# Kernel tuning notes

Measured on AMD Instinct MI355X. Metric: run time of the kernel, lower is better.

The kernel has to match this reference:

```python
import jax, jax.numpy as jnp
import numpy as np

T, N, C, S = 1600, 32, 512, 200
BLANK = 0
ALPHA = 0.5
NEG = -1e30  # finite stand-in for -inf (safe for grads)


def setup_inputs() -> dict:
    key = jax.random.key(0)
    k1, k2, k3 = jax.random.split(key, 3)
    # valid log-probabilities (log-softmax over vocab), shape (T, N, C)
    log_probs = jax.nn.log_softmax(jax.random.normal(k1, (T, N, C), jnp.float32), axis=-1)
    # labels in [1, C) so blank=0 never appears in targets
    targets = jax.random.randint(k2, (N, S), 1, C)
    input_lens = jnp.full((N,), T, dtype=jnp.int32)
    target_lens = jax.random.randint(k3, (N,), S // 2, S + 1)
    return {"log_probs": log_probs, "targets": targets,
            "input_lens": input_lens, "target_lens": target_lens}


def _ctc_forward(log_probs, targets, input_lens, target_lens):
    """Per-example CTC negative log-likelihood (reduction='none')."""
    Tt, Nn, Cc = log_probs.shape
    Ss = targets.shape[1]
    L = 2 * Ss + 1  # extended label sequence: blank, l1, blank, l2, ...

    ext = jnp.zeros((Nn, L), dtype=targets.dtype).at[:, 1::2].set(targets)  # (N, L)
    s_idx = jnp.arange(L)
    ext_m2 = jnp.pad(ext, ((0, 0), (2, 0)), constant_values=BLANK)[:, :L]
    # skip transition s-2 -> s allowed only for non-blank labels differing from s-2
    allow_skip = (ext != BLANK) & (ext != ext_m2) & (s_idx >= 2)[None, :]

    emit0 = jnp.take_along_axis(log_probs[0], ext, axis=1)  # (N, L)
    alpha0 = jnp.full((Nn, L), NEG, jnp.float32)
    alpha0 = alpha0.at[:, 0].set(emit0[:, 0])
    alpha0 = alpha0.at[:, 1].set(jnp.where(target_lens >= 1, emit0[:, 1], NEG))

    def step(alpha, xs):
        lp_t, t = xs  # lp_t: (N, C)
        emit = jnp.take_along_axis(lp_t, ext, axis=1)  # (N, L)
        a1 = jnp.pad(alpha, ((0, 0), (1, 0)), constant_values=NEG)[:, :L]
        a2 = jnp.where(allow_skip,
                       jnp.pad(alpha, ((0, 0), (2, 0)), constant_values=NEG)[:, :L],
                       NEG)
        m = jnp.maximum(jnp.maximum(alpha, a1), a2)
        new = m + jnp.log(jnp.exp(alpha - m) + jnp.exp(a1 - m) + jnp.exp(a2 - m)) + emit
        active = (t < input_lens)[:, None]  # freeze trellis past input_len
        return jnp.where(active, new, alpha), None

    alpha, _ = jax.lax.scan(step, alpha0, (log_probs[1:], jnp.arange(1, Tt)))

    idx_last = (2 * target_lens).astype(jnp.int32)  # final blank position
    idx_prev = jnp.maximum(idx_last - 1, 0)  # final label position
    a_last = jnp.take_along_axis(alpha, idx_last[:, None], axis=1)[:, 0]
    a_prev = jnp.where(target_lens > 0,
                       jnp.take_along_axis(alpha, idx_prev[:, None], axis=1)[:, 0],
                       NEG)
    return -jnp.logaddexp(a_last, a_prev)  # (N,)


def reference(log_probs, targets, input_lens, target_lens):
    per_ex = _ctc_forward(log_probs, targets, input_lens, target_lens)
    # zero_infinity=True: zero out infeasible alignments
    per_ex = jnp.where(per_ex < 1e29, per_ex, 0.0)
    norm = jnp.maximum(target_lens.astype(jnp.float32), 1.0) ** ALPHA
    return jnp.mean(per_ex / norm)
```

## Files before the change

kernel.cpp:

```cpp
#include <hip/hip_runtime.h>

#define T_DIM 1600
#define N_DIM 32
#define C_DIM 512
#define S_DIM 200
#define RCP_LN2 1.44269504088896340736f
#define LN2F 0.69314718055994530942f
#define ESENT (-(1 << 28))

static __device__ __forceinline__ float fast_exp2(float x) {
#if __has_builtin(__builtin_amdgcn_exp2f)
    return __builtin_amdgcn_exp2f(x);
#else
    return exp2f(x);
#endif
}

static __device__ __forceinline__ float fast_log2(float x) {
#if __has_builtin(__builtin_amdgcn_logf)
    return __builtin_amdgcn_logf(x);
#else
    return log2f(x);
#endif
}

static __device__ __forceinline__ float dpp_shr1_f(float x) {
    return __int_as_float(__builtin_amdgcn_update_dpp(
        0, __float_as_int(x), 0x138, 0xf, 0xf, false));
}
static __device__ __forceinline__ int dpp_shr1_i(int x, int old0) {
    return __builtin_amdgcn_update_dpp(old0, x, 0x138, 0xf, 0xf, false);
}
static __device__ __forceinline__ int dpp_prefix_max_i(int x) {
    int t;
    t = __builtin_amdgcn_update_dpp(x, x, 0x111, 0xf, 0xf, false); x = (t > x) ? t : x;
    t = __builtin_amdgcn_update_dpp(x, x, 0x112, 0xf, 0xf, false); x = (t > x) ? t : x;
    t = __builtin_amdgcn_update_dpp(x, x, 0x114, 0xf, 0xf, false); x = (t > x) ? t : x;
    t = __builtin_amdgcn_update_dpp(x, x, 0x118, 0xf, 0xf, false); x = (t > x) ? t : x;
    t = __builtin_amdgcn_update_dpp(x, x, 0x142, 0xf, 0xf, false); x = (t > x) ? t : x;
    t = __builtin_amdgcn_update_dpp(x, x, 0x143, 0xf, 0xf, false); x = (t > x) ? t : x;
    return x;
}

static __device__ __forceinline__ void gl_lds16(const float* g, float* l) {
    __builtin_amdgcn_global_load_lds(
        (const __attribute__((address_space(1))) unsigned int*)g,
        (__attribute__((address_space(3))) unsigned int*)l, 16, 0, 0);
}

#define VMWAIT16() __builtin_amdgcn_s_waitcnt(0x4F70)

__global__ __launch_bounds__(64) void ctc_dp(
    const float* __restrict__ lp, const int* __restrict__ tgts,
    const int* __restrict__ input_lens, const int* __restrict__ target_lens,
    float* __restrict__ out, float* __restrict__ ws)
{
    __shared__ float rows[3][8][C_DIM];

    const int blk = blockIdx.x;
    const int n = blk >> 1;
    const int role = blk & 1;
    const int lane = threadIdx.x & 63;
    const int* tgt = tgts + n * S_DIM;

    int len = input_lens[n];
    if (len > T_DIM) len = T_DIM;
    const int lenc = (len < 1) ? 1 : len;
    const int tl = target_lens[n];
    const int mid = (lenc + 1) >> 1;
    const int nsb = lenc - mid;

    float* afin_g = ws + 64 + (size_t)n * 1152;
    float* bfin_g = afin_g + 512;
    int* escF_g = (int*)(afin_g + 1024);
    int* escB_g = escF_g + 64;
    int* counter = (int*)ws + n;

#define TMAP_F(ti_) ((ti_) > mid - 1 ? mid - 1 : (ti_))
#define TMAP_B(ti_) (lenc - 1 - (ti_) < 0 ? 0 : lenc - 1 - (ti_))

#define ISSUE(B_, c_, TMAP_) do {                                             \
        int tb_ = (c_) * 8;                                                   \
        _Pragma("unroll")                                                     \
        for (int r_ = 0; r_ < 8; ++r_) {                                      \
            int ti_ = tb_ + r_;                                               \
            int t_ = TMAP_(ti_);                                              \
            const float* g_ = lp + ((size_t)t_ * N_DIM + n) * C_DIM + lane*4; \
            gl_lds16(g_,       &rows[(B_)][r_][0]);                           \
            gl_lds16(g_ + 256, &rows[(B_)][r_][256]);                         \
        }                                                                     \
    } while (0)

#define GATHER_RAW(B_, LAB_, qb_, q1_, q3_, q5_, q7_) do {                    \
        _Pragma("unroll")                                                     \
        for (int r_ = 0; r_ < 8; ++r_) {                                      \
            qb_[r_] = rows[(B_)][r_][0];                                      \
            q1_[r_] = rows[(B_)][r_][LAB_[0]];                                \
            q3_[r_] = rows[(B_)][r_][LAB_[1]];                                \
            q5_[r_] = rows[(B_)][r_][LAB_[2]];                                \
            q7_[r_] = rows[(B_)][r_][LAB_[3]];                                \
        }                                                                     \
    } while (0)

#define BOUNDARY() do {                                                       \
        float lm_ = fmaxf(fmaxf(fmaxf(a0, a1), fmaxf(a2, a3)),                \
                          fmaxf(fmaxf(a4, a5), fmaxf(a6, a7)));               \
        bool nz_ = (lm_ > 0.0f);                                              \
        int kl_ = (int)((__float_as_uint(lm_) >> 23) & 0xffu) - 127;          \
        int prop_ = nz_ ? (E + kl_) : ESENT;                                  \
        int g_ = dpp_prefix_max_i(prop_ + 32 * lane);                         \
        int Efin_ = g_ - 32 * lane;                                           \
        if (nz_) {                                                            \
            int sh_ = E - Efin_;                                              \
            int h1_ = sh_ / 2, h2_ = sh_ - h1_;                               \
            float f_ = fast_exp2((float)h1_), gg_ = fast_exp2((float)h2_);    \
            float fg_ = f_ * gg_;                                             \
            a0 *= fg_; a1 *= fg_; a2 *= fg_; a3 *= fg_;                       \
            a4 *= fg_; a5 *= fg_; a6 *= fg_; a7 *= fg_;                       \
        }                                                                     \
        int Eprev_ = dpp_shr1_i(Efin_, ESENT);                                \
        E = Efin_;                                                            \
        if (lane == 0) {                                                      \
            scale_d = 0.0f;                                                   \
        } else {                                                              \
            int d_ = Eprev_ - Efin_;               \
            scale_d = (d_ < -126) ? 0.0f : fast_exp2((float)d_);              \
        }                                                                     \
    } while (0)

#define COMPUTE_F(c8_, FIRST_, qb_, q1_, q3_, q5_, q7_) do {                  \
        _Pragma("unroll")                                                     \
        for (int r_ = 0; r_ < 8; ++r_) {                                      \
            int t_ = (c8_) + r_;                                              \
            if (t_ >= mid) break;                                             \
            float pb_ = fast_exp2(qb_[r_] * RCP_LN2);                         \
            float p1_ = fast_exp2(q1_[r_] * RCP_LN2);                         \
            float p3_ = fast_exp2(q3_[r_] * RCP_LN2);                         \
            float p5_ = fast_exp2(q5_[r_] * RCP_LN2);                         \
            float p7_ = fast_exp2(q7_[r_] * RCP_LN2);                         \
            if ((FIRST_) && r_ == 0) {                                        \
                if (lane == 0) {                                              \
                    a0 = pb_;                                                 \
                    a1 = (tl >= 1) ? p1_ : 0.0f;                              \
                }                                                             \
            } else {                                                          \
                float P_ = dpp_shr1_f(a7) * scale_d;                          \
                float n0_ = (a0 + P_) * pb_;                                  \
                float n1_ = fmaf(sk[0], P_,  a1 + a0) * p1_;                  \
                float n2_ = (a2 + a1) * pb_;                                  \
                float n3_ = fmaf(sk[1], a1, a3 + a2) * p3_;                   \
                float n4_ = (a4 + a3) * pb_;                                  \
                float n5_ = fmaf(sk[2], a3, a5 + a4) * p5_;                   \
                float n6_ = (a6 + a5) * pb_;                                  \
                float n7_ = fmaf(sk[3], a5, a7 + a6) * p7_;                   \
                a0 = n0_; a1 = n1_; a2 = n2_; a3 = n3_;                       \
                a4 = n4_; a5 = n5_; a6 = n6_; a7 = n7_;                       \
            }                                                                 \
        }                                                                     \
    } while (0)

#define COMPUTE_B(c8_, qb_, q1_, q3_, q5_, q7_) do {                          \
        _Pragma("unroll")                                                     \
        for (int r_ = 0; r_ < 8; ++r_) {                                      \
            int ti_ = (c8_) + r_;                                             \
            if (ti_ >= nsb) break;                                            \
            float pb_ = fast_exp2(qb_[r_] * RCP_LN2);                         \
            float p1_ = fast_exp2(q1_[r_] * RCP_LN2);                         \
            float p3_ = fast_exp2(q3_[r_] * RCP_LN2);                         \
            float p5_ = fast_exp2(q5_[r_] * RCP_LN2);                         \
            float p7_ = fast_exp2(q7_[r_] * RCP_LN2);                         \
            float c0_ = pb_ * a0, c1_ = p1_ * a1;                             \
            float c2_ = pb_ * a2, c3_ = p3_ * a3;                             \
            float c4_ = pb_ * a4, c5_ = p5_ * a5;                             \
            float c6_ = pb_ * a6, c7_ = p7_ * a7;                             \
            float P_ = dpp_shr1_f(c7_) * scale_d;                             \
            a0 = c0_ + P_;                                                    \
            a1 = fmaf(aH[0], P_,  c1_ + c0_);                                 \
            a2 = c2_ + c1_;                                                   \
            a3 = fmaf(aH[1], c1_, c3_ + c2_);                                 \
            a4 = c4_ + c3_;                                                   \
            a5 = fmaf(aH[2], c3_, c5_ + c4_);                                 \
            a6 = c6_ + c5_;                                                   \
            a7 = fmaf(aH[3], c5_, c7_ + c6_);                                 \
        }                                                                     \
    } while (0)

#define PHASE_F(k_, GB_, GS_, CS_, IB_, F_) do {                              \
        VMWAIT16();                                                           \
        GATHER_RAW(GB_, labidx, qb##GS_, q1##GS_, q3##GS_, q5##GS_, q7##GS_); \
        COMPUTE_F((k_) * 8, F_, qb##CS_, q1##CS_, q3##CS_, q5##CS_, q7##CS_); \
        BOUNDARY();                                                           \
        ISSUE(IB_, (k_) + 3, TMAP_F);                                         \
    } while (0)

#define PHASE_B(k_, GB_, GS_, CS_, IB_) do {                                  \
        VMWAIT16();                                                           \
        GATHER_RAW(GB_, labH, qb##GS_, q1##GS_, q3##GS_, q5##GS_, q7##GS_);   \
        COMPUTE_B((k_) * 8, qb##CS_, q1##CS_, q3##CS_, q5##CS_, q7##CS_);     \
        BOUNDARY();                                                           \
        ISSUE(IB_, (k_) + 3, TMAP_B);                                         \
    } while (0)

    if (role == 0) {
        int labidx[4];
        float sk[4];
#pragma unroll
        for (int jj = 0; jj < 4; ++jj) {
            int s = lane * 8 + 2 * jj + 1;
            int i = (s - 1) >> 1;
            int lab = 0;
            float al = 0.0f;
            if (i < S_DIM) {
                lab = tgt[i];
                if (s >= 3 && i >= 1) al = (tgt[i] != tgt[i - 1]) ? 1.0f : 0.0f;
            }
            if (lab < 0 || lab >= C_DIM) lab = 0;
            labidx[jj] = lab;
            sk[jj] = al;
        }

        float a0 = 0.0f, a1 = 0.0f, a2 = 0.0f, a3 = 0.0f;
        float a4 = 0.0f, a5 = 0.0f, a6 = 0.0f, a7 = 0.0f;
        int E = 0;
        float scale_d = (lane == 0) ? 0.0f : 1.0f;
        float qbA[8], q1A[8], q3A[8], q5A[8], q7A[8];
        float qbB[8], q1B[8], q3B[8], q5B[8], q7B[8];

        ISSUE(0, 0, TMAP_F);
        ISSUE(1, 1, TMAP_F);
        VMWAIT16();
        GATHER_RAW(0, labidx, qbA, q1A, q3A, q5A, q7A);
        ISSUE(2, 2, TMAP_F);

        const int ncf = (mid + 7) >> 3;
        const int kmaxf = ((ncf + 5) / 6) * 6;
        for (int k6 = 0; k6 < kmaxf; k6 += 6) {
            bool f0 = (k6 == 0);
            PHASE_F(k6 + 0, 1, B, A, 0, f0);
            PHASE_F(k6 + 1, 2, A, B, 1, false);
            PHASE_F(k6 + 2, 0, B, A, 2, false);
            PHASE_F(k6 + 3, 1, A, B, 0, false);
            PHASE_F(k6 + 4, 2, B, A, 1, false);
            PHASE_F(k6 + 5, 0, A, B, 2, false);
        }

        float4 lo = make_float4(a0, a1, a2, a3);
        float4 hi = make_float4(a4, a5, a6, a7);
        reinterpret_cast<float4*>(afin_g)[lane * 2] = lo;
        reinterpret_cast<float4*>(afin_g)[lane * 2 + 1] = hi;
        escF_g[lane] = E;
    } else {
        int labH[4];
        float aH[4];
#pragma unroll
        for (int jj = 0; jj < 4; ++jj) {
            int shat = lane * 8 + 2 * jj + 1;
            int s = 510 - shat;
            int lab = 0;
            float al = 0.0f;
            if (s >= 1 && s <= 399) {
                lab = tgt[(s - 1) >> 1];
                if (s + 2 <= 400) al = (tgt[(s + 1) >> 1] != tgt[(s - 1) >> 1]) ? 1.0f : 0.0f;
            }
            if (lab < 0 || lab >= C_DIM) lab = 0;
            labH[jj] = lab;
            aH[jj] = al;
        }

        float a0, a1, a2, a3, a4, a5, a6, a7;
#define BINIT(aj_, j_) do {                                                   \
            int s_ = 510 - (lane * 8 + (j_));                                 \
            aj_ = (s_ == 2 * tl || (tl > 0 && s_ == 2 * tl - 1)) ? 1.0f : 0.0f; \
        } while (0)
        BINIT(a0, 0); BINIT(a1, 1); BINIT(a2, 2); BINIT(a3, 3);
        BINIT(a4, 4); BINIT(a5, 5); BINIT(a6, 6); BINIT(a7, 7);
#undef BINIT
        int E = 0;
        float scale_d = (lane == 0) ? 0.0f : 1.0f;
        float qbA[8], q1A[8], q3A[8], q5A[8], q7A[8];
        float qbB[8], q1B[8], q3B[8], q5B[8], q7B[8];

        ISSUE(0, 0, TMAP_B);
        ISSUE(1, 1, TMAP_B);
        VMWAIT16();
        GATHER_RAW(0, labH, qbA, q1A, q3A, q5A, q7A);
        ISSUE(2, 2, TMAP_B);

        const int ncb = (nsb + 7) >> 3;
        const int kmaxb = ((ncb + 5) / 6) * 6;
        for (int k6 = 0; k6 < kmaxb; k6 += 6) {
            PHASE_B(k6 + 0, 1, B, A, 0);
            PHASE_B(k6 + 1, 2, A, B, 1);
            PHASE_B(k6 + 2, 0, B, A, 2);
            PHASE_B(k6 + 3, 1, A, B, 0);
            PHASE_B(k6 + 4, 2, B, A, 1);
            PHASE_B(k6 + 5, 0, A, B, 2);
        }

        float4 lo = make_float4(a0, a1, a2, a3);
        float4 hi = make_float4(a4, a5, a6, a7);
        reinterpret_cast<float4*>(bfin_g)[lane * 2] = lo;
        reinterpret_cast<float4*>(bfin_g)[lane * 2 + 1] = hi;
        escB_g[lane] = E;
    }

    __threadfence();
    int prev = 0;
    if (lane == 0)
        prev = __hip_atomic_fetch_add(counter, 1, __ATOMIC_ACQ_REL,
                                      __HIP_MEMORY_SCOPE_AGENT);
    prev = __shfl(prev, 0);
    if (prev != 1) return;

    __threadfence();

    {
        const int l = lane;
        const int Ef = escF_g[l];
        float m8 = -1e30f, s8 = 0.0f;
#pragma unroll
        for (int j = 0; j < 8; ++j) {
            int s = 8 * l + j;
            float x = -1e30f;
            if (s <= 400) {
                float af = afin_g[s];
                int shat = 510 - s;
                float bf = bfin_g[shat];
                if (af > 0.0f && bf > 0.0f)
                    x = fast_log2(af) + fast_log2(bf) + (float)(Ef + escB_g[shat >> 3]);
            }
            float m2 = fmaxf(m8, x);
            s8 = s8 * fast_exp2(m8 - m2) + fast_exp2(x - m2);
            m8 = m2;
        }
        float M = m8, V = s8;
#pragma unroll
        for (int off = 1; off < 64; off <<= 1) {
            float Mo = __shfl_xor(M, off);
            float Vo = __shfl_xor(V, off);
            float Mn = fmaxf(M, Mo);
            V = V * fast_exp2(M - Mn) + Vo * fast_exp2(Mo - Mn);
            M = Mn;
        }
        if (l == 0) {
            float X = M + fast_log2(V);
            float per_ex = -LN2F * X;
            if (!(per_ex < 1e29f)) per_ex = 0.0f;
            float tlf = (float)tl;
            if (tlf < 1.0f) tlf = 1.0f;
            atomicAdd(out, per_ex / sqrtf(tlf) * (1.0f / N_DIM));
        }
    }
#undef ISSUE
#undef GATHER_RAW
#undef BOUNDARY
#undef COMPUTE_F
#undef COMPUTE_B
#undef PHASE_F
#undef PHASE_B
#undef TMAP_F
#undef TMAP_B
}

extern "C" void kernel_launch(void* const* d_in, const int* in_sizes, int n_in,
                              void* d_out, int out_size, void* d_ws, size_t ws_size,
                              hipStream_t stream) {
    (void)in_sizes; (void)n_in; (void)ws_size;
    const float* lp   = (const float*)d_in[0];
    const int* tgts   = (const int*)d_in[1];
    const int* ilens  = (const int*)d_in[2];
    const int* tlens  = (const int*)d_in[3];

    hipMemsetAsync(d_out, 0, (size_t)out_size * sizeof(float), stream);
    hipMemsetAsync(d_ws, 0, N_DIM * sizeof(int), stream);
    ctc_dp<<<2 * N_DIM, 64, 0, stream>>>(lp, tgts, ilens, tlens,
                                         (float*)d_out, (float*)d_ws);
}
```

Baseline: 248.8 us.

## Split CTC recurrence into producer and consumer wavefronts with LDS handoff

```diff
diff --git a/kernel.cpp b/kernel.cpp
--- a/kernel.cpp
+++ b/kernel.cpp
@@ -48,19 +48,29 @@
         (__attribute__((address_space(3))) unsigned int*)l, 16, 0, 0);
 }
 
-#define VMWAIT16() __builtin_amdgcn_s_waitcnt(0x4F70)
-
-__global__ __launch_bounds__(64) void ctc_dp(
+#define VMWAIT8()  __builtin_amdgcn_s_waitcnt(0x0F78)
+#define VMDRAIN()  __builtin_amdgcn_s_waitcnt(0x0F70)
+#define PHASE_SYNC() do {                                                     \
+        __builtin_amdgcn_sched_barrier(0);                                    \
+        __builtin_amdgcn_s_waitcnt(0xC07F);              \
+        __builtin_amdgcn_s_barrier();                                         \
+        __builtin_amdgcn_sched_barrier(0);                                    \
+    } while (0)
+
+__global__ __launch_bounds__(192) void ctc_dp(
     const float* __restrict__ lp, const int* __restrict__ tgts,
     const int* __restrict__ input_lens, const int* __restrict__ target_lens,
     float* __restrict__ out, float* __restrict__ ws)
 {
     __shared__ float rows[3][8][C_DIM];
+    __shared__ float slab[2][5][8][64];
 
     const int blk = blockIdx.x;
     const int n = blk >> 1;
     const int role = blk & 1;
-    const int lane = threadIdx.x & 63;
+    const int tid = threadIdx.x;
+    const int wid = tid >> 6;
+    const int lane = tid & 63;
     const int* tgt = tgts + n * S_DIM;
 
     int len = input_lens[n];
@@ -69,6 +79,8 @@
     const int tl = target_lens[n];
     const int mid = (lenc + 1) >> 1;
     const int nsb = lenc - mid;
+    const int nsteps = (role == 0) ? mid : nsb;
+    const int nc = (nsteps + 7) >> 3;
 
     float* afin_g = ws + 64 + (size_t)n * 1152;
     float* bfin_g = afin_g + 512;
@@ -76,29 +88,78 @@
     int* escB_g = escF_g + 64;
     int* counter = (int*)ws + n;
 
-#define TMAP_F(ti_) ((ti_) > mid - 1 ? mid - 1 : (ti_))
-#define TMAP_B(ti_) (lenc - 1 - (ti_) < 0 ? 0 : lenc - 1 - (ti_))
-
-#define ISSUE(B_, c_, TMAP_) do {                                             \
-        int tb_ = (c_) * 8;                                                   \
-        _Pragma("unroll")                                                     \
-        for (int r_ = 0; r_ < 8; ++r_) {                                      \
-            int ti_ = tb_ + r_;                                               \
-            int t_ = TMAP_(ti_);                                              \
+    int lab[4];
+    float skh[4];
+    if (role == 0) {
+#pragma unroll
+        for (int jj = 0; jj < 4; ++jj) {
+            int s = lane * 8 + 2 * jj + 1;
+            int i = (s - 1) >> 1;
+            int lb = 0;
+            float al = 0.0f;
+            if (i < S_DIM) {
+                lb = tgt[i];
+                if (s >= 3 && i >= 1) al = (tgt[i] != tgt[i - 1]) ? 1.0f : 0.0f;
+            }
+            if (lb < 0 || lb >= C_DIM) lb = 0;
+            lab[jj] = lb;
+            skh[jj] = al;
+        }
+    } else {
+#pragma unroll
+        for (int jj = 0; jj < 4; ++jj) {
+            int shat = lane * 8 + 2 * jj + 1;
+            int s = 510 - shat;
+            int lb = 0;
+            float al = 0.0f;
+            if (s >= 1 && s <= 399) {
+                lb = tgt[(s - 1) >> 1];
+                if (s + 2 <= 400) al = (tgt[(s + 1) >> 1] != tgt[(s - 1) >> 1]) ? 1.0f : 0.0f;
+            }
+            if (lb < 0 || lb >= C_DIM) lb = 0;
+            lab[jj] = lb;
+            skh[jj] = al;
+        }
+    }
+
+    const int r0 = (wid == 1) ? 0 : 4;
+
+    auto tmap = [&](int ti) -> int {
+        if (role == 0) return ti > mid - 1 ? mid - 1 : ti;
+        int t = lenc - 1 - ti;
+        return t < 0 ? 0 : t;
+    };
+
+#define STAGE(B_, c_) do {                                                    \
+        _Pragma("unroll")                                                     \
+        for (int rr_ = 0; rr_ < 4; ++rr_) {                                   \
+            int r_ = r0 + rr_;                                                \
+            int t_ = tmap((c_) * 8 + r_);                                     \
             const float* g_ = lp + ((size_t)t_ * N_DIM + n) * C_DIM + lane*4; \
             gl_lds16(g_,       &rows[(B_)][r_][0]);                           \
             gl_lds16(g_ + 256, &rows[(B_)][r_][256]);                         \
         }                                                                     \
     } while (0)
 
-#define GATHER_RAW(B_, LAB_, qb_, q1_, q3_, q5_, q7_) do {                    \
-        _Pragma("unroll")                                                     \
-        for (int r_ = 0; r_ < 8; ++r_) {                                      \
-            qb_[r_] = rows[(B_)][r_][0];                                      \
-            q1_[r_] = rows[(B_)][r_][LAB_[0]];                                \
-            q3_[r_] = rows[(B_)][r_][LAB_[1]];                                \
-            q5_[r_] = rows[(B_)][r_][LAB_[2]];                                \
-            q7_[r_] = rows[(B_)][r_][LAB_[3]];                                \
+#define CONV(B_, S_) do {                                                     \
+        float v_[20];                                                         \
+        _Pragma("unroll")                                                     \
+        for (int rr_ = 0; rr_ < 4; ++rr_) {                                   \
+            int r_ = r0 + rr_;                                                \
+            v_[rr_ * 5 + 0] = rows[(B_)][r_][0];                              \
+            v_[rr_ * 5 + 1] = rows[(B_)][r_][lab[0]];                         \
+            v_[rr_ * 5 + 2] = rows[(B_)][r_][lab[1]];                         \
+            v_[rr_ * 5 + 3] = rows[(B_)][r_][lab[2]];                         \
+            v_[rr_ * 5 + 4] = rows[(B_)][r_][lab[3]];                         \
+        }                                                                     \
+        __builtin_amdgcn_sched_barrier(0);                                    \
+        _Pragma("unroll")                                                     \
+        for (int rr_ = 0; rr_ < 4; ++rr_) {                                   \
+            int r_ = r0 + rr_;                                                \
+            _Pragma("unroll")                                                 \
+            for (int j_ = 0; j_ < 5; ++j_)                                    \
+                slab[(S_)][j_][r_][lane] =                                    \
+                    fast_exp2(v_[rr_ * 5 + j_] * RCP_LN2);                    \
         }                                                                     \
     } while (0)
 
@@ -128,16 +189,23 @@
         }                                                                     \
     } while (0)
 
-#define COMPUTE_F(c8_, FIRST_, qb_, q1_, q3_, q5_, q7_) do {                  \
+#define CONSUME_F(c8_, S_, FIRST_) do {                                       \
+        float q_[40];                                                         \
+        _Pragma("unroll")                                                     \
+        for (int r_ = 0; r_ < 8; ++r_)                                        \
+            _Pragma("unroll")                                                 \
+            for (int j_ = 0; j_ < 5; ++j_)                                    \
+                q_[r_ * 5 + j_] = slab[(S_)][j_][r_][lane];                   \
+        __builtin_amdgcn_sched_barrier(0);                                    \
         _Pragma("unroll")                                                     \
         for (int r_ = 0; r_ < 8; ++r_) {                                      \
             int t_ = (c8_) + r_;                                              \
             if (t_ >= mid) break;                                             \
-            float pb_ = fast_exp2(qb_[r_] * RCP_LN2);                         \
-            float p1_ = fast_exp2(q1_[r_] * RCP_LN2);                         \
-            float p3_ = fast_exp2(q3_[r_] * RCP_LN2);                         \
-            float p5_ = fast_exp2(q5_[r_] * RCP_LN2);                         \
-            float p7_ = fast_exp2(q7_[r_] * RCP_LN2);                         \
+            float pb_ = q_[r_ * 5 + 0];                                       \
+            float p1_ = q_[r_ * 5 + 1];                                       \
+            float p3_ = q_[r_ * 5 + 2];                                       \
+            float p5_ = q_[r_ * 5 + 3];                                       \
+            float p7_ = q_[r_ * 5 + 4];                                       \
             if ((FIRST_) && r_ == 0) {                                        \
                 if (lane == 0) {                                              \
                     a0 = pb_;                                                 \
@@ -146,128 +214,65 @@
             } else {                                                          \
                 float P_ = dpp_shr1_f(a7) * scale_d;                          \
                 float n0_ = (a0 + P_) * pb_;                                  \
-                float n1_ = fmaf(sk[0], P_,  a1 + a0) * p1_;                  \
+                float n1_ = fmaf(skh[0], P_,  a1 + a0) * p1_;                 \
                 float n2_ = (a2 + a1) * pb_;                                  \
-                float n3_ = fmaf(sk[1], a1, a3 + a2) * p3_;                   \
+                float n3_ = fmaf(skh[1], a1, a3 + a2) * p3_;                  \
                 float n4_ = (a4 + a3) * pb_;                                  \
-                float n5_ = fmaf(sk[2], a3, a5 + a4) * p5_;                   \
+                float n5_ = fmaf(skh[2], a3, a5 + a4) * p5_;                  \
                 float n6_ = (a6 + a5) * pb_;                                  \
-                float n7_ = fmaf(sk[3], a5, a7 + a6) * p7_;                   \
+                float n7_ = fmaf(skh[3], a5, a7 + a6) * p7_;                  \
                 a0 = n0_; a1 = n1_; a2 = n2_; a3 = n3_;                       \
                 a4 = n4_; a5 = n5_; a6 = n6_; a7 = n7_;                       \
             }                                                                 \
         }                                                                     \
     } while (0)
 
-#define COMPUTE_B(c8_, qb_, q1_, q3_, q5_, q7_) do {                          \
+#define CONSUME_B(c8_, S_) do {                                               \
+        float q_[40];                                                         \
+        _Pragma("unroll")                                                     \
+        for (int r_ = 0; r_ < 8; ++r_)                                        \
+            _Pragma("unroll")                                                 \
+            for (int j_ = 0; j_ < 5; ++j_)                                    \
+                q_[r_ * 5 + j_] = slab[(S_)][j_][r_][lane];                   \
+        __builtin_amdgcn_sched_barrier(0);                                    \
         _Pragma("unroll")                                                     \
         for (int r_ = 0; r_ < 8; ++r_) {                                      \
             int ti_ = (c8_) + r_;                                             \
             if (ti_ >= nsb) break;                                            \
-            float pb_ = fast_exp2(qb_[r_] * RCP_LN2);                         \
-            float p1_ = fast_exp2(q1_[r_] * RCP_LN2);                         \
-            float p3_ = fast_exp2(q3_[r_] * RCP_LN2);                         \
-            float p5_ = fast_exp2(q5_[r_] * RCP_LN2);                         \
-            float p7_ = fast_exp2(q7_[r_] * RCP_LN2);                         \
+            float pb_ = q_[r_ * 5 + 0];                                       \
+            float p1_ = q_[r_ * 5 + 1];                                       \
+            float p3_ = q_[r_ * 5 + 2];                                       \
+            float p5_ = q_[r_ * 5 + 3];                                       \
+            float p7_ = q_[r_ * 5 + 4];                                       \
             float c0_ = pb_ * a0, c1_ = p1_ * a1;                             \
             float c2_ = pb_ * a2, c3_ = p3_ * a3;                             \
             float c4_ = pb_ * a4, c5_ = p5_ * a5;                             \
             float c6_ = pb_ * a6, c7_ = p7_ * a7;                             \
             float P_ = dpp_shr1_f(c7_) * scale_d;                             \
             a0 = c0_ + P_;                                                    \
-            a1 = fmaf(aH[0], P_,  c1_ + c0_);                                 \
+            a1 = fmaf(skh[0], P_,  c1_ + c0_);                                \
             a2 = c2_ + c1_;                                                   \
-            a3 = fmaf(aH[1], c1_, c3_ + c2_);                                 \
+            a3 = fmaf(skh[1], c1_, c3_ + c2_);                                \
             a4 = c4_ + c3_;                                                   \
-            a5 = fmaf(aH[2], c3_, c5_ + c4_);                                 \
+            a5 = fmaf(skh[2], c3_, c5_ + c4_);                                \
             a6 = c6_ + c5_;                                                   \
-            a7 = fmaf(aH[3], c5_, c7_ + c6_);                                 \
-        }                                                                     \
-    } while (0)
-
-#define PHASE_F(k_, GB_, GS_, CS_, IB_, F_) do {                              \
-        VMWAIT16();                                                           \
-        GATHER_RAW(GB_, labidx, qb##GS_, q1##GS_, q3##GS_, q5##GS_, q7##GS_); \
-        COMPUTE_F((k_) * 8, F_, qb##CS_, q1##CS_, q3##CS_, q5##CS_, q7##CS_); \
-        BOUNDARY();                                                           \
-        ISSUE(IB_, (k_) + 3, TMAP_F);                                         \
-    } while (0)
-
-#define PHASE_B(k_, GB_, GS_, CS_, IB_) do {                                  \
-        VMWAIT16();                                                           \
-        GATHER_RAW(GB_, labH, qb##GS_, q1##GS_, q3##GS_, q5##GS_, q7##GS_);   \
-        COMPUTE_B((k_) * 8, qb##CS_, q1##CS_, q3##CS_, q5##CS_, q7##CS_);     \
-        BOUNDARY();                                                           \
-        ISSUE(IB_, (k_) + 3, TMAP_B);                                         \
-    } while (0)
-
+            a7 = fmaf(skh[3], c5_, c7_ + c6_);                                \
+        }                                                                     \
+    } while (0)
+
+    if (wid >= 1) {
+        STAGE(0, 0);
+        STAGE(1, 1);
+        VMWAIT8();
+        CONV(0, 0);
+        STAGE(2, 2);
+    }
+    PHASE_SYNC();
+
+    float a0, a1, a2, a3, a4, a5, a6, a7;
     if (role == 0) {
-        int labidx[4];
-        float sk[4];
-#pragma unroll
-        for (int jj = 0; jj < 4; ++jj) {
-            int s = lane * 8 + 2 * jj + 1;
-            int i = (s - 1) >> 1;
-            int lab = 0;
-            float al = 0.0f;
-            if (i < S_DIM) {
-                lab = tgt[i];
-                if (s >= 3 && i >= 1) al = (tgt[i] != tgt[i - 1]) ? 1.0f : 0.0f;
-            }
-            if (lab < 0 || lab >= C_DIM) lab = 0;
-            labidx[jj] = lab;
-            sk[jj] = al;
-        }
-
-        float a0 = 0.0f, a1 = 0.0f, a2 = 0.0f, a3 = 0.0f;
-        float a4 = 0.0f, a5 = 0.0f, a6 = 0.0f, a7 = 0.0f;
-        int E = 0;
-        float scale_d = (lane == 0) ? 0.0f : 1.0f;
-        float qbA[8], q1A[8], q3A[8], q5A[8], q7A[8];
-        float qbB[8], q1B[8], q3B[8], q5B[8], q7B[8];
-
-        ISSUE(0, 0, TMAP_F);
-        ISSUE(1, 1, TMAP_F);
-        VMWAIT16();
-        GATHER_RAW(0, labidx, qbA, q1A, q3A, q5A, q7A);
-        ISSUE(2, 2, TMAP_F);
-
-        const int ncf = (mid + 7) >> 3;
-        const int kmaxf = ((ncf + 5) / 6) * 6;
-        for (int k6 = 0; k6 < kmaxf; k6 += 6) {
-            bool f0 = (k6 == 0);
-            PHASE_F(k6 + 0, 1, B, A, 0, f0);
-            PHASE_F(k6 + 1, 2, A, B, 1, false);
-            PHASE_F(k6 + 2, 0, B, A, 2, false);
-            PHASE_F(k6 + 3, 1, A, B, 0, false);
-            PHASE_F(k6 + 4, 2, B, A, 1, false);
-            PHASE_F(k6 + 5, 0, A, B, 2, false);
-        }
-
-        float4 lo = make_float4(a0, a1, a2, a3);
-        float4 hi = make_float4(a4, a5, a6, a7);
-        reinterpret_cast<float4*>(afin_g)[lane * 2] = lo;
-        reinterpret_cast<float4*>(afin_g)[lane * 2 + 1] = hi;
-        escF_g[lane] = E;
+        a0 = a1 = a2 = a3 = a4 = a5 = a6 = a7 = 0.0f;
     } else {
-        int labH[4];
-        float aH[4];
-#pragma unroll
-        for (int jj = 0; jj < 4; ++jj) {
-            int shat = lane * 8 + 2 * jj + 1;
-            int s = 510 - shat;
-            int lab = 0;
-            float al = 0.0f;
-            if (s >= 1 && s <= 399) {
-                lab = tgt[(s - 1) >> 1];
-                if (s + 2 <= 400) al = (tgt[(s + 1) >> 1] != tgt[(s - 1) >> 1]) ? 1.0f : 0.0f;
-            }
-            if (lab < 0 || lab >= C_DIM) lab = 0;
-            labH[jj] = lab;
-            aH[jj] = al;
-        }
-
-        float a0, a1, a2, a3, a4, a5, a6, a7;
 #define BINIT(aj_, j_) do {                                                   \
             int s_ = 510 - (lane * 8 + (j_));                                 \
             aj_ = (s_ == 2 * tl || (tl > 0 && s_ == 2 * tl - 1)) ? 1.0f : 0.0f; \
@@ -275,33 +280,45 @@
         BINIT(a0, 0); BINIT(a1, 1); BINIT(a2, 2); BINIT(a3, 3);
         BINIT(a4, 4); BINIT(a5, 5); BINIT(a6, 6); BINIT(a7, 7);
 #undef BINIT
-        int E = 0;
-        float scale_d = (lane == 0) ? 0.0f : 1.0f;
-        float qbA[8], q1A[8], q3A[8], q5A[8], q7A[8];
-        float qbB[8], q1B[8], q3B[8], q5B[8], q7B[8];
-
-        ISSUE(0, 0, TMAP_B);
-        ISSUE(1, 1, TMAP_B);
-        VMWAIT16();
-        GATHER_RAW(0, labH, qbA, q1A, q3A, q5A, q7A);
-        ISSUE(2, 2, TMAP_B);
-
-        const int ncb = (nsb + 7) >> 3;
-        const int kmaxb = ((ncb + 5) / 6) * 6;
-        for (int k6 = 0; k6 < kmaxb; k6 += 6) {
-            PHASE_B(k6 + 0, 1, B, A, 0);
-            PHASE_B(k6 + 1, 2, A, B, 1);
-            PHASE_B(k6 + 2, 0, B, A, 2);
-            PHASE_B(k6 + 3, 1, A, B, 0);
-            PHASE_B(k6 + 4, 2, B, A, 1);
-            PHASE_B(k6 + 5, 0, A, B, 2);
-        }
-
+    }
+    int E = 0;
+    float scale_d = (lane == 0) ? 0.0f : 1.0f;
+
+    int bg = 1, bi = 0, sw = 1, sr = 0;
+    for (int k = 0; k < nc; ++k) {
+        if (wid >= 1) {
+            VMWAIT8();
+            CONV(bg, sw);
+            STAGE(bi, k + 3);
+        } else {
+            if (role == 0) { CONSUME_F(k * 8, sr, (k == 0)); }
+            else           { CONSUME_B(k * 8, sr); }
+            BOUNDARY();
+        }
+        PHASE_SYNC();
+        bg = (bg == 2) ? 0 : bg + 1;
+        bi = (bi == 2) ? 0 : bi + 1;
+        sw ^= 1;
+        sr ^= 1;
+    }
+
+    if (wid >= 1) {
+        VMDRAIN();
+        return;
+    }
+
+    {
         float4 lo = make_float4(a0, a1, a2, a3);
         float4 hi = make_float4(a4, a5, a6, a7);
-        reinterpret_cast<float4*>(bfin_g)[lane * 2] = lo;
-        reinterpret_cast<float4*>(bfin_g)[lane * 2 + 1] = hi;
-        escB_g[lane] = E;
+        if (role == 0) {
+            reinterpret_cast<float4*>(afin_g)[lane * 2] = lo;
+            reinterpret_cast<float4*>(afin_g)[lane * 2 + 1] = hi;
+            escF_g[lane] = E;
+        } else {
+            reinterpret_cast<float4*>(bfin_g)[lane * 2] = lo;
+            reinterpret_cast<float4*>(bfin_g)[lane * 2 + 1] = hi;
+            escB_g[lane] = E;
+        }
     }
 
     __threadfence();
@@ -351,15 +368,11 @@
             atomicAdd(out, per_ex / sqrtf(tlf) * (1.0f / N_DIM));
         }
     }
-#undef ISSUE
-#undef GATHER_RAW
+#undef STAGE
+#undef CONV
 #undef BOUNDARY
-#undef COMPUTE_F
-#undef COMPUTE_B
-#undef PHASE_F
-#undef PHASE_B
-#undef TMAP_F
-#undef TMAP_B
+#undef CONSUME_F
+#undef CONSUME_B
 }
 
 extern "C" void kernel_launch(void* const* d_in, const int* in_sizes, int n_in,
@@ -373,6 +386,6 @@
 
     hipMemsetAsync(d_out, 0, (size_t)out_size * sizeof(float), stream);
     hipMemsetAsync(d_ws, 0, N_DIM * sizeof(int), stream);
-    ctc_dp<<<2 * N_DIM, 64, 0, stream>>>(lp, tgts, ilens, tlens,
-                                         (float*)d_out, (float*)d_ws);
-}
+    ctc_dp<<<2 * N_DIM, 192, 0, stream>>>(lp, tgts, ilens, tlens,
+                                          (float*)d_out, (float*)d_ws);
+}
```

Result: faster. 230.2 us (-7.5%).
